# Performance work log

Measured on AMD Instinct MI355X. Metric: run time of the kernel, lower is better.

The kernel has to match this reference:

```python
import jax, jax.numpy as jnp
import numpy as np

NEG_SLOPE = 0.2  # PyG GATConv default leaky_relu slope


def _gat_conv(x, src, dst, W, a_src, a_dst, b, num_nodes):
    # Linear transform: [N, F_out]
    h = x @ W
    # Per-node attention halves (heads=1): [N]
    alpha_s = h @ a_src
    alpha_d = h @ a_dst
    # Per-edge raw score for edge j->i: a_src.h_j + a_dst.h_i
    e = jax.nn.leaky_relu(alpha_s[src] + alpha_d[dst], NEG_SLOPE)
    # Softmax over edges grouped by destination node (numerically stable)
    m = jax.ops.segment_max(e, dst, num_segments=num_nodes)
    ex = jnp.exp(e - m[dst])
    denom = jax.ops.segment_sum(ex, dst, num_segments=num_nodes)
    coef = ex / denom[dst]
    # Attention-weighted aggregation of source features into destinations
    out = jax.ops.segment_sum(h[src] * coef[:, None], dst, num_segments=num_nodes)
    return out + b


def setup_inputs() -> dict:
    key = jax.random.key(0)
    ks = jax.random.split(key, 12)
    N, F_in, F_hid, F_out, E = 100000, 128, 64, 40, 1600000
    x = jax.random.normal(ks[0], (N, F_in), dtype=jnp.float32)
    edge_index = jax.random.randint(ks[1], (2, E), 0, N, dtype=jnp.int64)
    g = lambda k, shape, fan: jax.random.normal(k, shape, dtype=jnp.float32) * (1.0 / np.sqrt(fan))
    return {
        "x": x,
        "edge_index": edge_index,
        "W1": g(ks[2], (F_in, F_hid), F_in),
        "a_src1": g(ks[3], (F_hid,), F_hid),
        "a_dst1": g(ks[4], (F_hid,), F_hid),
        "b1": jnp.zeros((F_hid,), dtype=jnp.float32),
        "W2": g(ks[5], (F_hid, F_out), F_hid),
        "a_src2": g(ks[6], (F_out,), F_out),
        "a_dst2": g(ks[7], (F_out,), F_out),
        "b2": jnp.zeros((F_out,), dtype=jnp.float32),
    }


def reference(x, edge_index, W1, a_src1, a_dst1, b1, W2, a_src2, a_dst2, b2):
    N = x.shape[0]
    # PyG GATConv adds self loops by default
    loops = jnp.arange(N, dtype=edge_index.dtype)
    src = jnp.concatenate([edge_index[0], loops])
    dst = jnp.concatenate([edge_index[1], loops])
    h = _gat_conv(x, src, dst, W1, a_src1, a_dst1, b1, N)
    h = jax.nn.relu(h)
    # dropout p=0.5 is inactive in eval mode
    h = _gat_conv(h, src, dst, W2, a_src2, a_dst2, b2, N)
    return jax.nn.log_softmax(h, axis=-1)
```

## Files before the change

kernel.cpp:

```cpp
#include <hip/hip_runtime.h>
#include <math.h>


constexpr int F_IN = 128;
constexpr int F_H  = 64;
constexpr int F_O  = 40;
constexpr int NBMAX = 512;
constexpr int CHUNK = 8192;

using h2 = decltype(__builtin_amdgcn_cvt_pkrtz(0.f, 0.f));
typedef __attribute__((ext_vector_type(4))) float f32x4;
typedef __attribute__((ext_vector_type(8))) short s16x8;

__device__ __forceinline__ h2 u2h(unsigned u) { return __builtin_bit_cast(h2, u); }

__device__ __forceinline__ float fdot2f(h2 a, h2 b, float c) {
#if __has_builtin(__builtin_amdgcn_fdot2)
    return __builtin_amdgcn_fdot2(a, b, c, false);
#else
    return c + (float)a.x * (float)b.x + (float)a.y * (float)b.y;
#endif
}
__device__ __forceinline__ h2 pklo(unsigned a, unsigned b) {
    return u2h(__builtin_amdgcn_perm(a, b, 0x05040100u));
}
__device__ __forceinline__ h2 pkhi(unsigned a, unsigned b) {
    return u2h(__builtin_amdgcn_perm(a, b, 0x07060302u));
}
__device__ __forceinline__ unsigned short f2h(float f) {
    _Float16 x = (_Float16)f;
    return __builtin_bit_cast(unsigned short, x);
}


__global__ __launch_bounds__(256) void k_binA(const int* __restrict__ dsts,
                                              int* __restrict__ bcnt,
                                              int E, int Et, int NB) {
    __shared__ int hist[NBMAX];
    for (int i = threadIdx.x; i < NB; i += 256) hist[i] = 0;
    __syncthreads();
    int e0 = blockIdx.x * 2048;
#pragma unroll
    for (int it = 0; it < 8; ++it) {
        int e = e0 + it * 256 + threadIdx.x;
        if (e < Et) {
            int d = (e < E) ? dsts[e] : (e - E);
            atomicAdd(&hist[d >> 8], 1);
        }
    }
    __syncthreads();
    for (int i = threadIdx.x; i < NB; i += 256) {
        int c = hist[i];
        if (c) atomicAdd(&bcnt[i], c);
    }
}

__global__ __launch_bounds__(NBMAX) void k_binB(const int* __restrict__ bcnt,
                                                int* __restrict__ bbase,
                                                int* __restrict__ bcur,
                                                int* __restrict__ rp,
                                                int NB, int N, int Et) {
    __shared__ int sc[NBMAX];
    int t = threadIdx.x;
    int v = (t < NB) ? bcnt[t] : 0;
    sc[t] = v; __syncthreads();
    int x = v;
    for (int o = 1; o < NBMAX; o <<= 1) {
        int y = (t >= o) ? sc[t - o] : 0;
        __syncthreads();
        x += y;
        sc[t] = x;
        __syncthreads();
    }
    if (t < NB) { int b = x - v; bbase[t] = b; bcur[t] = b; }
    if (t == 0) rp[N] = Et;
}

__global__ __launch_bounds__(256) void k_binC(const int* __restrict__ srcs,
                                              const int* __restrict__ dsts,
                                              int* __restrict__ bcur,
                                              unsigned* __restrict__ binned,
                                              int E, int Et, int NB) {
    __shared__ int hist[NBMAX];
    __shared__ int gbase[NBMAX];
    __shared__ int lcnt[NBMAX];
    int t = threadIdx.x;
    for (int i = t; i < NB; i += 256) hist[i] = 0;
    __syncthreads();
    int e0 = blockIdx.x * CHUNK;
#pragma unroll 4
    for (int it = 0; it < CHUNK / 256; ++it) {
        int e = e0 + it * 256 + t;
        if (e < Et) {
            int d = (e < E) ? dsts[e] : (e - E);
            atomicAdd(&hist[d >> 8], 1);
        }
    }
    __syncthreads();
    for (int i = t; i < NB; i += 256) {
        int c = hist[i];
        gbase[i] = c ? atomicAdd(&bcur[i], c) : 0;
        lcnt[i] = 0;
    }
    __syncthreads();
#pragma unroll 4
    for (int it = 0; it < CHUNK / 256; ++it) {
        int e = e0 + it * 256 + t;
        if (e < Et) {
            int s, d;
            if (e < E) { s = srcs[e]; d = dsts[e]; } else { s = e - E; d = s; }
            int b = d >> 8;
            int p = atomicAdd(&lcnt[b], 1);
            binned[gbase[b] + p] = (unsigned)s | ((unsigned)(d & 255) << 24);
        }
    }
}

__global__ __launch_bounds__(256) void k_binD(const unsigned* __restrict__ binned,
                                              const int* __restrict__ bbase,
                                              const int* __restrict__ bcur,
                                              int* __restrict__ rp,
                                              int* __restrict__ csr, int N) {
    __shared__ int hist[256];
    __shared__ int sc[256];
    __shared__ int lcnt[256];
    int b = blockIdx.x, t = threadIdx.x;
    int base = bbase[b], end = bcur[b];
    hist[t] = 0; __syncthreads();
    for (int j = base + t; j < end; j += 256)
        atomicAdd(&hist[binned[j] >> 24], 1);
    __syncthreads();
    int v = hist[t];
    sc[t] = v; __syncthreads();
    int x = v;
    for (int o = 1; o < 256; o <<= 1) {
        int y = (t >= o) ? sc[t - o] : 0;
        __syncthreads();
        x += y;
        sc[t] = x;
        __syncthreads();
    }
    int pref = x - v;
    int g = (b << 8) + t;
    if (g < N) rp[g] = base + pref;
    sc[t] = pref;
    lcnt[t] = 0;
    __syncthreads();
    for (int j = base + t; j < end; j += 256) {
        unsigned w = binned[j];
        int v2 = (int)(w >> 24);
        int s = (int)(w & 0xFFFFFFu);
        int p = atomicAdd(&lcnt[v2], 1);
        csr[base + sc[v2] + p] = s;
    }
}


__global__ __launch_bounds__(256) void k_wsplit(const float* __restrict__ W,
                                                unsigned short* __restrict__ WhiT,
                                                unsigned short* __restrict__ WloT) {
    int i = blockIdx.x * 256 + threadIdx.x;
    if (i >= F_IN * F_H) return;
    int k = i >> 6, c = i & 63;
    float w = W[i];
    unsigned u = __float_as_uint(w);
    unsigned hi = u & 0xFFFF0000u;
    float d = w - __uint_as_float(hi);
    WhiT[c * F_IN + k] = (unsigned short)(hi >> 16);
    WloT[c * F_IN + k] = (unsigned short)(__float_as_uint(d) >> 16);
}


__global__ __launch_bounds__(256) void k_gemm1m(const float* __restrict__ x,
                                                const unsigned short* __restrict__ WhiT,
                                                const unsigned short* __restrict__ WloT,
                                                const float* __restrict__ avs,
                                                const float* __restrict__ avd,
                                                unsigned short* __restrict__ h,
                                                float* __restrict__ as,
                                                float* __restrict__ ad, int N) {
    __shared__ unsigned short hs[64][72];
    const int t = threadIdx.x;
    const int wv = t >> 6;
    const int lane = t & 63;
    const int lrow = lane & 15;
    const int lk8 = lane >> 4;
    const int r0 = blockIdx.x * 64;
    const int arow = r0 + wv * 16 + lrow;
    const float* xp = x + (size_t)min(arow, N - 1) * F_IN;

    float4 xv0[4], xv1[4];
#pragma unroll
    for (int kt = 0; kt < 4; ++kt) {
        xv0[kt] = *(const float4*)&xp[kt * 32 + lk8 * 8];
        xv1[kt] = *(const float4*)&xp[kt * 32 + lk8 * 8 + 4];
    }
    s16x8 ah[4], al[4];
#pragma unroll
    for (int kt = 0; kt < 4; ++kt) {
        float e0[8] = {xv0[kt].x, xv0[kt].y, xv0[kt].z, xv0[kt].w,
                       xv1[kt].x, xv1[kt].y, xv1[kt].z, xv1[kt].w};
        unsigned uh[4], ul[4];
#pragma unroll
        for (int p = 0; p < 4; ++p) {
            float a0 = e0[2 * p], a1 = e0[2 * p + 1];
            unsigned u0 = __float_as_uint(a0), u1 = __float_as_uint(a1);
            float d0 = a0 - __uint_as_float(u0 & 0xFFFF0000u);
            float d1 = a1 - __uint_as_float(u1 & 0xFFFF0000u);
            uh[p] = __builtin_amdgcn_perm(u1, u0, 0x07060302u);
            ul[p] = __builtin_amdgcn_perm(__float_as_uint(d1), __float_as_uint(d0), 0x07060302u);
        }
        ah[kt] = __builtin_bit_cast(s16x8, make_uint4(uh[0], uh[1], uh[2], uh[3]));
        al[kt] = __builtin_bit_cast(s16x8, make_uint4(ul[0], ul[1], ul[2], ul[3]));
    }

    f32x4 acc[4] = {};
#pragma unroll
    for (int kt = 0; kt < 4; ++kt) {
#pragma unroll
        for (int ct = 0; ct < 4; ++ct) {
            const int boff = (ct * 16 + lrow) * F_IN + kt * 32 + lk8 * 8;
            s16x8 bh = *(const s16x8*)&WhiT[boff];
            s16x8 bl = *(const s16x8*)&WloT[boff];
            acc[ct] = __builtin_amdgcn_mfma_f32_16x16x32_bf16(ah[kt], bh, acc[ct], 0, 0, 0);
            acc[ct] = __builtin_amdgcn_mfma_f32_16x16x32_bf16(al[kt], bh, acc[ct], 0, 0, 0);
            acc[ct] = __builtin_amdgcn_mfma_f32_16x16x32_bf16(ah[kt], bl, acc[ct], 0, 0, 0);
        }
    }

    float avs_c[4], avd_c[4];
#pragma unroll
    for (int ct = 0; ct < 4; ++ct) {
        avs_c[ct] = avs[ct * 16 + lrow];
        avd_c[ct] = avd[ct * 16 + lrow];
    }
#pragma unroll
    for (int r = 0; r < 4; ++r) {
        float ps = acc[0][r] * avs_c[0] + acc[1][r] * avs_c[1]
                 + acc[2][r] * avs_c[2] + acc[3][r] * avs_c[3];
        float pd = acc[0][r] * avd_c[0] + acc[1][r] * avd_c[1]
                 + acc[2][r] * avd_c[2] + acc[3][r] * avd_c[3];
#pragma unroll
        for (int o = 8; o; o >>= 1) {
            ps += __shfl_xor(ps, o, 16);
            pd += __shfl_xor(pd, o, 16);
        }
        int orow = r0 + wv * 16 + lk8 * 4 + r;
        if (lrow == 0 && orow < N) { as[orow] = ps; ad[orow] = pd; }
    }

#pragma unroll
    for (int ct = 0; ct < 4; ++ct)
#pragma unroll
        for (int r = 0; r < 4; ++r)
            hs[wv * 16 + lk8 * 4 + r][ct * 16 + lrow] = f2h(acc[ct][r]);
    __syncthreads();
    const int row = t >> 2, ch = t & 3;
    const int grow = r0 + row;
    if (grow < N) {
        uint4 v0 = *(const uint4*)&hs[row][ch * 16];
        uint4 v1 = *(const uint4*)&hs[row][ch * 16 + 8];
        uint4* gp = (uint4*)(h + (size_t)grow * F_H + ch * 16);
        gp[0] = v0; gp[1] = v1;
    }
}


__global__ __launch_bounds__(256) void k_gemm2(const float* __restrict__ xin,
                                               const float* __restrict__ W,
                                               const float* __restrict__ avs,
                                               const float* __restrict__ avd,
                                               unsigned short* __restrict__ h,
                                               float* __restrict__ as,
                                               float* __restrict__ ad, int N) {
    __shared__ __align__(16) float Ws[F_H * F_O];
    for (int i = threadIdx.x; i < F_H * F_O; i += 256) Ws[i] = W[i];
    __syncthreads();
    int t = threadIdx.x;
    int r0 = blockIdx.x * 64 + (t >> 3) * 2;
    int l = t & 7;
    if (r0 >= N) return;
    const float4* xa = (const float4*)(xin + (size_t)r0 * F_H);
    const float4* xb = (const float4*)(xin + (size_t)(r0 + 1) * F_H);
    float acca[5] = {}, accb[5] = {};
#pragma unroll
    for (int k4 = 0; k4 < F_H / 4; ++k4) {
        float4 xva = xa[k4];
        float4 xvb = xb[k4];
        int kb = k4 * 4;
#pragma unroll
        for (int kk = 0; kk < 4; ++kk) {
            const float* wr = &Ws[(kb + kk) * F_O + l];
            float w0 = wr[0], w1 = wr[8], w2 = wr[16], w3 = wr[24], w4 = wr[32];
            float xs = (&xva.x)[kk];
            acca[0] += xs * w0; acca[1] += xs * w1; acca[2] += xs * w2;
            acca[3] += xs * w3; acca[4] += xs * w4;
            float ys = (&xvb.x)[kk];
            accb[0] += ys * w0; accb[1] += ys * w1; accb[2] += ys * w2;
            accb[3] += ys * w3; accb[4] += ys * w4;
        }
    }
    float psa = 0.f, pda = 0.f, psb = 0.f, pdb = 0.f;
    unsigned short* ra = h + (size_t)r0 * F_H;
    unsigned short* rb = h + (size_t)(r0 + 1) * F_H;
#pragma unroll
    for (int cc = 0; cc < 5; ++cc) {
        int c = l + 8 * cc;
        ra[c] = f2h(acca[cc]);
        rb[c] = f2h(accb[cc]);
        float vs = avs[c], vd = avd[c];
        psa += acca[cc] * vs; pda += acca[cc] * vd;
        psb += accb[cc] * vs; pdb += accb[cc] * vd;
    }
#pragma unroll
    for (int pp = 0; pp < 3; ++pp) {
        int c = 40 + l * 3 + pp;
        ra[c] = 0; rb[c] = 0;
    }
#pragma unroll
    for (int o = 4; o; o >>= 1) {
        psa += __shfl_xor(psa, o, 8);
        pda += __shfl_xor(pda, o, 8);
        psb += __shfl_xor(psb, o, 8);
        pdb += __shfl_xor(pdb, o, 8);
    }
    if (l == 0) { as[r0] = psa; ad[r0] = pda; as[r0 + 1] = psb; ad[r0 + 1] = pdb; }
}


template <int FOUT, bool RELU, bool LOGSM>
__global__ __launch_bounds__(256) void k_agg(const int* __restrict__ rp,
                                             const int* __restrict__ csr,
                                             const float* __restrict__ as,
                                             const float* __restrict__ ad,
                                             const uint4* __restrict__ h4,
                                             const float* __restrict__ bias,
                                             float* __restrict__ out, int N) {
    constexpr int CAP = 64;
    __shared__ __align__(16) uint2 wsb[4][8][CAP + 2];
    const int w = threadIdx.x >> 6;
    const int g = (threadIdx.x >> 3) & 7;
    const int c = threadIdx.x & 7;
    const int i = blockIdx.x * 32 + (threadIdx.x >> 3);
    if (i >= N) return;
    const int start = rp[i], end = rp[i + 1];
    const int deg = end - start;
    const int dm = min(deg, CAP);
    const float adi = ad[i];

    for (int idx = c; idx < dm; idx += 8) {
        int srcn = csr[start + idx];
        float e = as[srcn] + adi;
        e = fmaxf(e, 0.2f * e);
        wsb[w][g][idx] = make_uint2(__float_as_uint(__expf(e)), (unsigned)srcn);
    }
    if (c == 0 && (dm & 1))
        wsb[w][g][dm] = make_uint2(0u, (unsigned)i);

    const uint4* pw = (const uint4*)wsb[w][g];
    float acc[8] = {};
    float sacc = 0.f;
    const int npair = (dm + 1) >> 1;
    for (int p = 0; p < npair; ++p) {
        uint4 t = pw[p];
        float w0 = __uint_as_float(t.x), w1 = __uint_as_float(t.z);
        sacc += w0 + w1;
        uint4 hv0 = h4[((unsigned)t.y << 3) + c];
        uint4 hv1 = h4[((unsigned)t.w << 3) + c];
        h2 wp = __builtin_amdgcn_cvt_pkrtz(w0, w1);
        acc[0] = fdot2f(wp, pklo(hv1.x, hv0.x), acc[0]);
        acc[1] = fdot2f(wp, pkhi(hv1.x, hv0.x), acc[1]);
        acc[2] = fdot2f(wp, pklo(hv1.y, hv0.y), acc[2]);
        acc[3] = fdot2f(wp, pkhi(hv1.y, hv0.y), acc[3]);
        acc[4] = fdot2f(wp, pklo(hv1.z, hv0.z), acc[4]);
        acc[5] = fdot2f(wp, pkhi(hv1.z, hv0.z), acc[5]);
        acc[6] = fdot2f(wp, pklo(hv1.w, hv0.w), acc[6]);
        acc[7] = fdot2f(wp, pkhi(hv1.w, hv0.w), acc[7]);
    }

    for (int j = start + dm; j < end; ++j) {
        int srcn = csr[j];
        float e = as[srcn] + adi;
        e = fmaxf(e, 0.2f * e);
        float wv = __expf(e);
        sacc += wv;
        uint4 hv = h4[((unsigned)srcn << 3) + c];
        h2 wp = __builtin_amdgcn_cvt_pkrtz(wv, 0.f);
        acc[0] = fdot2f(wp, pklo(hv.x, hv.x), acc[0]);
        acc[1] = fdot2f(wp, pkhi(hv.x, hv.x), acc[1]);
        acc[2] = fdot2f(wp, pklo(hv.y, hv.y), acc[2]);
        acc[3] = fdot2f(wp, pkhi(hv.y, hv.y), acc[3]);
        acc[4] = fdot2f(wp, pklo(hv.z, hv.z), acc[4]);
        acc[5] = fdot2f(wp, pkhi(hv.z, hv.z), acc[5]);
        acc[6] = fdot2f(wp, pklo(hv.w, hv.w), acc[6]);
        acc[7] = fdot2f(wp, pkhi(hv.w, hv.w), acc[7]);
    }

    float inv = 1.f / sacc;

    if (!LOGSM) {
        float r[8];
#pragma unroll
        for (int k = 0; k < 8; ++k) {
            r[k] = fmaf(acc[k], inv, bias[8 * c + k]);
            if (RELU) r[k] = fmaxf(r[k], 0.f);
        }
        float4* op = (float4*)(out + (size_t)i * FOUT + 8 * c);
        op[0] = make_float4(r[0], r[1], r[2], r[3]);
        op[1] = make_float4(r[4], r[5], r[6], r[7]);
    } else {
        constexpr int VC = FOUT / 8;
        bool act = (c < VC);
        float v[8];
#pragma unroll
        for (int k = 0; k < 8; ++k) {
            float bv = bias[act ? 8 * c + k : 0];
            v[k] = act ? fmaf(acc[k], inv, bv) : -INFINITY;
        }
        float mx = v[0];
#pragma unroll
        for (int k = 1; k < 8; ++k) mx = fmaxf(mx, v[k]);
#pragma unroll
        for (int o = 1; o <= 4; o <<= 1) mx = fmaxf(mx, __shfl_xor(mx, o));
        float es = 0.f;
        if (act) {
#pragma unroll
            for (int k = 0; k < 8; ++k) es += __expf(v[k] - mx);
        }
#pragma unroll
        for (int o = 1; o <= 4; o <<= 1) es += __shfl_xor(es, o);
        if (act) {
            float lse = mx + __logf(es);
            float4* op = (float4*)(out + (size_t)i * FOUT + 8 * c);
            op[0] = make_float4(v[0] - lse, v[1] - lse, v[2] - lse, v[3] - lse);
            op[1] = make_float4(v[4] - lse, v[5] - lse, v[6] - lse, v[7] - lse);
        }
    }
}


extern "C" void kernel_launch(void* const* d_in, const int* in_sizes, int n_in,
                              void* d_out, int out_size, void* d_ws, size_t ws_size,
                              hipStream_t stream) {
    const float* x   = (const float*)d_in[0];
    const int* edges = (const int*)d_in[1];
    const float* W1  = (const float*)d_in[2];
    const float* av_s1 = (const float*)d_in[3];
    const float* av_d1 = (const float*)d_in[4];
    const float* b1  = (const float*)d_in[5];
    const float* W2  = (const float*)d_in[6];
    const float* av_s2 = (const float*)d_in[7];
    const float* av_d2 = (const float*)d_in[8];
    const float* b2  = (const float*)d_in[9];
    float* out = (float*)d_out;

    const int N  = in_sizes[0] / F_IN;
    const int E  = in_sizes[1] / 2;
    const int Et = E + N;
    const int NB = (N + 255) >> 8;

    char* p = (char*)d_ws;
    auto alloc = [&](size_t bytes) {
        char* q = p;
        p += (bytes + 255) & ~(size_t)255;
        return (void*)q;
    };
    unsigned short* h1 = (unsigned short*)alloc((size_t)N * F_H * 2);
    float* out1   = (float*)alloc((size_t)N * F_H * 4);
    float* as1    = (float*)alloc((size_t)N * 4);
    float* ad1    = (float*)alloc((size_t)N * 4);
    float* as2    = (float*)alloc((size_t)N * 4);
    float* ad2    = (float*)alloc((size_t)N * 4);
    int* rp       = (int*)alloc((size_t)(N + 1) * 4);
    int* bcnt     = (int*)alloc(NBMAX * 4);
    int* bbase    = (int*)alloc(NBMAX * 4);
    int* bcur     = (int*)alloc(NBMAX * 4);
    unsigned* binned = (unsigned*)alloc((size_t)Et * 4);
    int* csr      = (int*)alloc((size_t)Et * 4);
    unsigned short* WhiT = (unsigned short*)alloc((size_t)F_H * F_IN * 2);
    unsigned short* WloT = (unsigned short*)alloc((size_t)F_H * F_IN * 2);
    (void)n_in; (void)out_size; (void)ws_size;

    const int* srcs = edges;
    const int* dsts = edges + E;

    hipMemsetAsync(bcnt, 0, NBMAX * 4, stream);

    k_wsplit<<<(F_IN * F_H + 255) / 256, 256, 0, stream>>>(W1, WhiT, WloT);
    k_binA<<<(Et + 2047) / 2048, 256, 0, stream>>>(dsts, bcnt, E, Et, NB);
    k_binB<<<1, NBMAX, 0, stream>>>(bcnt, bbase, bcur, rp, NB, N, Et);
    k_binC<<<(Et + CHUNK - 1) / CHUNK, 256, 0, stream>>>(srcs, dsts, bcur, binned, E, Et, NB);
    k_binD<<<NB, 256, 0, stream>>>(binned, bbase, bcur, rp, csr, N);

    k_gemm1m<<<(N + 63) / 64, 256, 0, stream>>>(x, WhiT, WloT, av_s1, av_d1, h1, as1, ad1, N);
    int gAgg = (N + 31) / 32;
    k_agg<F_H, true, false><<<gAgg, 256, 0, stream>>>(rp, csr, as1, ad1,
                                                      (const uint4*)h1, b1, out1, N);
    k_gemm2<<<(N + 63) / 64, 256, 0, stream>>>(out1, W2, av_s2, av_d2, h1, as2, ad2, N);
    k_agg<F_O, false, true><<<gAgg, 256, 0, stream>>>(rp, csr, as2, ad2,
                                                      (const uint4*)h1, b2, out, N);
}
```

Before: 296.0 us.

## Degree-sort nodes for aggregation, unroll gather by four, store layer-1 output as fp16

```diff
diff --git a/kernel.cpp b/kernel.cpp
--- a/kernel.cpp
+++ b/kernel.cpp
@@ -7,6 +7,7 @@
 constexpr int F_O  = 40;
 constexpr int NBMAX = 512;
 constexpr int CHUNK = 8192;
+constexpr int DCLS  = 64;
 
 using h2 = decltype(__builtin_amdgcn_cvt_pkrtz(0.f, 0.f));
 typedef __attribute__((ext_vector_type(4))) float f32x4;
@@ -153,6 +154,47 @@
         int p = atomicAdd(&lcnt[v2], 1);
         csr[base + sc[v2] + p] = s;
     }
+}
+
+
+__global__ __launch_bounds__(256) void k_dsortA(const int* __restrict__ rp,
+                                                int* __restrict__ dcnt, int N) {
+    __shared__ int h[DCLS];
+    if (threadIdx.x < DCLS) h[threadIdx.x] = 0;
+    __syncthreads();
+    int i = blockIdx.x * 256 + threadIdx.x;
+    if (i < N) {
+        int d = min(rp[i + 1] - rp[i], DCLS - 1);
+        atomicAdd(&h[d], 1);
+    }
+    __syncthreads();
+    if (threadIdx.x < DCLS) {
+        int c = h[threadIdx.x];
+        if (c) atomicAdd(&dcnt[threadIdx.x], c);
+    }
+}
+
+__global__ __launch_bounds__(64) void k_dsortB(const int* __restrict__ dcnt,
+                                               int* __restrict__ dcur) {
+    int t = threadIdx.x;
+    int v = dcnt[t];
+    int x = v;
+#pragma unroll
+    for (int o = 1; o < 64; o <<= 1) {
+        int y = __shfl_up(x, o);
+        if (t >= o) x += y;
+    }
+    dcur[t] = x - v;
+}
+
+__global__ __launch_bounds__(256) void k_dsortC(const int* __restrict__ rp,
+                                                int* __restrict__ dcur,
+                                                int* __restrict__ perm, int N) {
+    int i = blockIdx.x * 256 + threadIdx.x;
+    if (i >= N) return;
+    int d = min(rp[i + 1] - rp[i], DCLS - 1);
+    int p = atomicAdd(&dcur[d], 1);
+    perm[p] = i;
 }
 
 
@@ -266,7 +308,7 @@
 }
 
 
-__global__ __launch_bounds__(256) void k_gemm2(const float* __restrict__ xin,
+__global__ __launch_bounds__(256) void k_gemm2(const unsigned short* __restrict__ xin,
                                                const float* __restrict__ W,
                                                const float* __restrict__ avs,
                                                const float* __restrict__ avd,
@@ -280,22 +322,26 @@
     int r0 = blockIdx.x * 64 + (t >> 3) * 2;
     int l = t & 7;
     if (r0 >= N) return;
-    const float4* xa = (const float4*)(xin + (size_t)r0 * F_H);
-    const float4* xb = (const float4*)(xin + (size_t)(r0 + 1) * F_H);
+    const uint2* xa = (const uint2*)(xin + (size_t)r0 * F_H);
+    const uint2* xb = (const uint2*)(xin + (size_t)(r0 + 1) * F_H);
     float acca[5] = {}, accb[5] = {};
 #pragma unroll
     for (int k4 = 0; k4 < F_H / 4; ++k4) {
-        float4 xva = xa[k4];
-        float4 xvb = xb[k4];
+        uint2 ua = xa[k4];
+        uint2 ub = xb[k4];
+        h2 a01 = u2h(ua.x), a23 = u2h(ua.y);
+        h2 b01 = u2h(ub.x), b23 = u2h(ub.y);
+        float xva[4] = {(float)a01.x, (float)a01.y, (float)a23.x, (float)a23.y};
+        float xvb[4] = {(float)b01.x, (float)b01.y, (float)b23.x, (float)b23.y};
         int kb = k4 * 4;
 #pragma unroll
         for (int kk = 0; kk < 4; ++kk) {
             const float* wr = &Ws[(kb + kk) * F_O + l];
             float w0 = wr[0], w1 = wr[8], w2 = wr[16], w3 = wr[24], w4 = wr[32];
-            float xs = (&xva.x)[kk];
+            float xs = xva[kk];
             acca[0] += xs * w0; acca[1] += xs * w1; acca[2] += xs * w2;
             acca[3] += xs * w3; acca[4] += xs * w4;
-            float ys = (&xvb.x)[kk];
+            float ys = xvb[kk];
             accb[0] += ys * w0; accb[1] += ys * w1; accb[2] += ys * w2;
             accb[3] += ys * w3; accb[4] += ys * w4;
         }
@@ -328,24 +374,27 @@
 }
 
 
-template <int FOUT, bool RELU, bool LOGSM>
-__global__ __launch_bounds__(256) void k_agg(const int* __restrict__ rp,
+template <int FOUT, bool RELU, bool LOGSM, bool F16OUT>
+__global__ __launch_bounds__(256) void k_agg(const int* __restrict__ perm,
+                                             const int* __restrict__ rp,
                                              const int* __restrict__ csr,
                                              const float* __restrict__ as,
                                              const float* __restrict__ ad,
                                              const uint4* __restrict__ h4,
                                              const float* __restrict__ bias,
-                                             float* __restrict__ out, int N) {
+                                             void* __restrict__ outv, int N) {
     constexpr int CAP = 64;
     __shared__ __align__(16) uint2 wsb[4][8][CAP + 2];
     const int w = threadIdx.x >> 6;
     const int g = (threadIdx.x >> 3) & 7;
     const int c = threadIdx.x & 7;
-    const int i = blockIdx.x * 32 + (threadIdx.x >> 3);
-    if (i >= N) return;
+    const int slot = blockIdx.x * 32 + (threadIdx.x >> 3);
+    if (slot >= N) return;
+    const int i = perm[slot];
     const int start = rp[i], end = rp[i + 1];
     const int deg = end - start;
     const int dm = min(deg, CAP);
+    const int dmR4 = (dm + 3) & ~3;
     const float adi = ad[i];
 
     for (int idx = c; idx < dm; idx += 8) {
@@ -354,28 +403,43 @@
         e = fmaxf(e, 0.2f * e);
         wsb[w][g][idx] = make_uint2(__float_as_uint(__expf(e)), (unsigned)srcn);
     }
-    if (c == 0 && (dm & 1))
-        wsb[w][g][dm] = make_uint2(0u, (unsigned)i);
+    {
+        int idx = dm + c;
+        if (idx < dmR4) wsb[w][g][idx] = make_uint2(0u, (unsigned)i);
+    }
 
     const uint4* pw = (const uint4*)wsb[w][g];
-    float acc[8] = {};
+    float acc[8] = {}, acc2[8] = {};
     float sacc = 0.f;
-    const int npair = (dm + 1) >> 1;
-    for (int p = 0; p < npair; ++p) {
-        uint4 t = pw[p];
-        float w0 = __uint_as_float(t.x), w1 = __uint_as_float(t.z);
-        sacc += w0 + w1;
-        uint4 hv0 = h4[((unsigned)t.y << 3) + c];
-        uint4 hv1 = h4[((unsigned)t.w << 3) + c];
-        h2 wp = __builtin_amdgcn_cvt_pkrtz(w0, w1);
-        acc[0] = fdot2f(wp, pklo(hv1.x, hv0.x), acc[0]);
-        acc[1] = fdot2f(wp, pkhi(hv1.x, hv0.x), acc[1]);
-        acc[2] = fdot2f(wp, pklo(hv1.y, hv0.y), acc[2]);
-        acc[3] = fdot2f(wp, pkhi(hv1.y, hv0.y), acc[3]);
-        acc[4] = fdot2f(wp, pklo(hv1.z, hv0.z), acc[4]);
-        acc[5] = fdot2f(wp, pkhi(hv1.z, hv0.z), acc[5]);
-        acc[6] = fdot2f(wp, pklo(hv1.w, hv0.w), acc[6]);
-        acc[7] = fdot2f(wp, pkhi(hv1.w, hv0.w), acc[7]);
+    const int nquad = dmR4 >> 2;
+    for (int q = 0; q < nquad; ++q) {
+        uint4 t0 = pw[2 * q];
+        uint4 t1 = pw[2 * q + 1];
+        uint4 hv0 = h4[((unsigned)t0.y << 3) + c];
+        uint4 hv1 = h4[((unsigned)t0.w << 3) + c];
+        uint4 hv2 = h4[((unsigned)t1.y << 3) + c];
+        uint4 hv3 = h4[((unsigned)t1.w << 3) + c];
+        float w0 = __uint_as_float(t0.x), w1 = __uint_as_float(t0.z);
+        float w2 = __uint_as_float(t1.x), w3 = __uint_as_float(t1.z);
+        sacc += (w0 + w1) + (w2 + w3);
+        h2 wp0 = __builtin_amdgcn_cvt_pkrtz(w0, w1);
+        h2 wp1 = __builtin_amdgcn_cvt_pkrtz(w2, w3);
+        acc[0] = fdot2f(wp0, pklo(hv1.x, hv0.x), acc[0]);
+        acc[1] = fdot2f(wp0, pkhi(hv1.x, hv0.x), acc[1]);
+        acc[2] = fdot2f(wp0, pklo(hv1.y, hv0.y), acc[2]);
+        acc[3] = fdot2f(wp0, pkhi(hv1.y, hv0.y), acc[3]);
+        acc[4] = fdot2f(wp0, pklo(hv1.z, hv0.z), acc[4]);
+        acc[5] = fdot2f(wp0, pkhi(hv1.z, hv0.z), acc[5]);
+        acc[6] = fdot2f(wp0, pklo(hv1.w, hv0.w), acc[6]);
+        acc[7] = fdot2f(wp0, pkhi(hv1.w, hv0.w), acc[7]);
+        acc2[0] = fdot2f(wp1, pklo(hv3.x, hv2.x), acc2[0]);
+        acc2[1] = fdot2f(wp1, pkhi(hv3.x, hv2.x), acc2[1]);
+        acc2[2] = fdot2f(wp1, pklo(hv3.y, hv2.y), acc2[2]);
+        acc2[3] = fdot2f(wp1, pkhi(hv3.y, hv2.y), acc2[3]);
+        acc2[4] = fdot2f(wp1, pklo(hv3.z, hv2.z), acc2[4]);
+        acc2[5] = fdot2f(wp1, pkhi(hv3.z, hv2.z), acc2[5]);
+        acc2[6] = fdot2f(wp1, pklo(hv3.w, hv2.w), acc2[6]);
+        acc2[7] = fdot2f(wp1, pkhi(hv3.w, hv2.w), acc2[7]);
     }
 
     for (int j = start + dm; j < end; ++j) {
@@ -396,6 +460,8 @@
         acc[7] = fdot2f(wp, pkhi(hv.w, hv.w), acc[7]);
     }
 
+#pragma unroll
+    for (int k = 0; k < 8; ++k) acc[k] += acc2[k];
     float inv = 1.f / sacc;
 
     if (!LOGSM) {
@@ -405,10 +471,21 @@
             r[k] = fmaf(acc[k], inv, bias[8 * c + k]);
             if (RELU) r[k] = fmaxf(r[k], 0.f);
         }
-        float4* op = (float4*)(out + (size_t)i * FOUT + 8 * c);
-        op[0] = make_float4(r[0], r[1], r[2], r[3]);
-        op[1] = make_float4(r[4], r[5], r[6], r[7]);
+        if (F16OUT) {
+            unsigned short* oh = (unsigned short*)outv;
+            unsigned u0 = (unsigned)f2h(r[0]) | ((unsigned)f2h(r[1]) << 16);
+            unsigned u1 = (unsigned)f2h(r[2]) | ((unsigned)f2h(r[3]) << 16);
+            unsigned u2 = (unsigned)f2h(r[4]) | ((unsigned)f2h(r[5]) << 16);
+            unsigned u3 = (unsigned)f2h(r[6]) | ((unsigned)f2h(r[7]) << 16);
+            *(uint4*)(oh + (size_t)i * F_H + 8 * c) = make_uint4(u0, u1, u2, u3);
+        } else {
+            float* out = (float*)outv;
+            float4* op = (float4*)(out + (size_t)i * FOUT + 8 * c);
+            op[0] = make_float4(r[0], r[1], r[2], r[3]);
+            op[1] = make_float4(r[4], r[5], r[6], r[7]);
+        }
     } else {
+        float* out = (float*)outv;
         constexpr int VC = FOUT / 8;
         bool act = (c < VC);
         float v[8];
@@ -466,15 +543,18 @@
         return (void*)q;
     };
     unsigned short* h1 = (unsigned short*)alloc((size_t)N * F_H * 2);
-    float* out1   = (float*)alloc((size_t)N * F_H * 4);
+    unsigned short* out1h = (unsigned short*)alloc((size_t)N * F_H * 2);
     float* as1    = (float*)alloc((size_t)N * 4);
     float* ad1    = (float*)alloc((size_t)N * 4);
     float* as2    = (float*)alloc((size_t)N * 4);
     float* ad2    = (float*)alloc((size_t)N * 4);
     int* rp       = (int*)alloc((size_t)(N + 1) * 4);
+    int* perm     = (int*)alloc((size_t)N * 4);
     int* bcnt     = (int*)alloc(NBMAX * 4);
     int* bbase    = (int*)alloc(NBMAX * 4);
     int* bcur     = (int*)alloc(NBMAX * 4);
+    int* dcnt     = (int*)alloc(DCLS * 4);
+    int* dcur     = (int*)alloc(DCLS * 4);
     unsigned* binned = (unsigned*)alloc((size_t)Et * 4);
     int* csr      = (int*)alloc((size_t)Et * 4);
     unsigned short* WhiT = (unsigned short*)alloc((size_t)F_H * F_IN * 2);
@@ -485,6 +565,7 @@
     const int* dsts = edges + E;
 
     hipMemsetAsync(bcnt, 0, NBMAX * 4, stream);
+    hipMemsetAsync(dcnt, 0, DCLS * 4, stream);
 
     k_wsplit<<<(F_IN * F_H + 255) / 256, 256, 0, stream>>>(W1, WhiT, WloT);
     k_binA<<<(Et + 2047) / 2048, 256, 0, stream>>>(dsts, bcnt, E, Et, NB);
@@ -492,11 +573,16 @@
     k_binC<<<(Et + CHUNK - 1) / CHUNK, 256, 0, stream>>>(srcs, dsts, bcur, binned, E, Et, NB);
     k_binD<<<NB, 256, 0, stream>>>(binned, bbase, bcur, rp, csr, N);
 
+    int gN = (N + 255) / 256;
+    k_dsortA<<<gN, 256, 0, stream>>>(rp, dcnt, N);
+    k_dsortB<<<1, 64, 0, stream>>>(dcnt, dcur);
+    k_dsortC<<<gN, 256, 0, stream>>>(rp, dcur, perm, N);
+
     k_gemm1m<<<(N + 63) / 64, 256, 0, stream>>>(x, WhiT, WloT, av_s1, av_d1, h1, as1, ad1, N);
     int gAgg = (N + 31) / 32;
-    k_agg<F_H, true, false><<<gAgg, 256, 0, stream>>>(rp, csr, as1, ad1,
-                                                      (const uint4*)h1, b1, out1, N);
-    k_gemm2<<<(N + 63) / 64, 256, 0, stream>>>(out1, W2, av_s2, av_d2, h1, as2, ad2, N);
-    k_agg<F_O, false, true><<<gAgg, 256, 0, stream>>>(rp, csr, as2, ad2,
-                                                      (const uint4*)h1, b2, out, N);
-}
+    k_agg<F_H, true, false, true><<<gAgg, 256, 0, stream>>>(perm, rp, csr, as1, ad1,
+                                                            (const uint4*)h1, b1, out1h, N);
+    k_gemm2<<<(N + 63) / 64, 256, 0, stream>>>(out1h, W2, av_s2, av_d2, h1, as2, ad2, N);
+    k_agg<F_O, false, true, false><<<gAgg, 256, 0, stream>>>(perm, rp, csr, as2, ad2,
+                                                             (const uint4*)h1, b2, out, N);
+}
```

Result: slower. 586.5 us (+98.2%).
